# Performance work log

Measured on AMD Instinct MI355X. Metric: run time of the kernel, lower is better.

The kernel has to match this reference:

```python
import jax, jax.numpy as jnp
import numpy as np

N, E, IN, HID, H, G, CLS = 20000, 160000, 128, 96, 6, 512, 128
HD = H * HID  # heads * out_channels = 576
ARC_S = 30.0  # ArcFace scale (no margin at inference, no labels passed)


def _lin_params(key, fan_in, fan_out):
    k1, k2 = jax.random.split(key)
    lim = 1.0 / np.sqrt(fan_in)
    W = jax.random.uniform(k1, (fan_in, fan_out), minval=-lim, maxval=lim, dtype=jnp.float32)
    b = jax.random.uniform(k2, (fan_out,), minval=-lim, maxval=lim, dtype=jnp.float32)
    return W, b


def setup_inputs() -> dict:
    key = jax.random.key(0)
    ks = jax.random.split(key, 32)
    x = jax.random.normal(ks[0], (N, IN), dtype=jnp.float32)
    edge_index = jax.random.randint(ks[1], (2, E), 0, N, dtype=jnp.int64)
    batch = jnp.sort(jax.random.randint(ks[2], (N,), 0, G, dtype=jnp.int64))
    # conv1: IN -> HID (per-head dim HID, H heads)
    Wq1, bq1 = _lin_params(ks[3], IN, HD)
    Wk1, bk1 = _lin_params(ks[4], IN, HD)
    Wv1, bv1 = _lin_params(ks[5], IN, HD)
    Ws1, bs1 = _lin_params(ks[6], IN, HID)
    # convs 2..5 share shapes: HID -> HID, stacked on leading axis of 4
    def stack(fn_keys, fi, fo):
        Ws, bs = zip(*[_lin_params(k, fi, fo) for k in fn_keys])
        return jnp.stack(Ws), jnp.stack(bs)
    Wq_r, bq_r = stack(ks[7:11], HID, HD)
    Wk_r, bk_r = stack(ks[11:15], HID, HD)
    Wv_r, bv_r = stack(ks[15:19], HID, HD)
    Ws_r, bs_r = stack(ks[19:23], HID, HID)
    fc1_w, fc1_b = _lin_params(ks[23], HID, HID)
    fc2_w, fc2_b = _lin_params(ks[24], HID, HID)
    arc_w = jax.random.normal(ks[25], (CLS, HID), dtype=jnp.float32)
    return dict(x=x, edge_index=edge_index, batch=batch,
                Wq1=Wq1, bq1=bq1, Wk1=Wk1, bk1=bk1, Wv1=Wv1, bv1=bv1, Ws1=Ws1, bs1=bs1,
                Wq_r=Wq_r, bq_r=bq_r, Wk_r=Wk_r, bk_r=bk_r, Wv_r=Wv_r, bv_r=bv_r,
                Ws_r=Ws_r, bs_r=bs_r,
                fc1_w=fc1_w, fc1_b=fc1_b, fc2_w=fc2_w, fc2_b=fc2_b, arc_w=arc_w)


def transformer_conv(x, src, dst, Wq, bq, Wk, bk, Wv, bv, Ws, bs):
    n = x.shape[0]
    q = (x @ Wq + bq).reshape(n, H, HID)
    k = (x @ Wk + bk).reshape(n, H, HID)
    v = (x @ Wv + bv).reshape(n, H, HID)
    # edge-wise attention logits [E, H]
    alpha = jnp.einsum('ehd,ehd->eh', q[dst], k[src]) / jnp.sqrt(jnp.float32(HID))
    # segment softmax over incoming edges of each destination node
    m = jax.ops.segment_max(alpha, dst, num_segments=n)
    a = jnp.exp(alpha - m[dst])
    s = jax.ops.segment_sum(a, dst, num_segments=n)
    a = a / s[dst]
    out = jax.ops.segment_sum(a[:, :, None] * v[src], dst, num_segments=n)  # [n, H, HID]
    # concat=False -> mean over heads; root_weight skip connection
    return out.mean(axis=1) + x @ Ws + bs


def reference(x, edge_index, batch,
              Wq1, bq1, Wk1, bk1, Wv1, bv1, Ws1, bs1,
              Wq_r, bq_r, Wk_r, bk_r, Wv_r, bv_r, Ws_r, bs_r,
              fc1_w, fc1_b, fc2_w, fc2_b, arc_w):
    src, dst = edge_index[0], edge_index[1]
    h = jax.nn.relu(transformer_conv(x, src, dst, Wq1, bq1, Wk1, bk1, Wv1, bv1, Ws1, bs1))
    for i in range(4):  # gtconv2..gtconv5
        h = jax.nn.relu(transformer_conv(h, src, dst, Wq_r[i], bq_r[i], Wk_r[i], bk_r[i],
                                         Wv_r[i], bv_r[i], Ws_r[i], bs_r[i]))
    # global mean pool over graphs
    sums = jax.ops.segment_sum(h, batch, num_segments=G)
    cnt = jax.ops.segment_sum(jnp.ones((h.shape[0], 1), h.dtype), batch, num_segments=G)
    g = sums / jnp.maximum(cnt, 1.0)
    g = jax.nn.relu(g @ fc1_w + fc1_b)
    g = jax.nn.relu(g @ fc2_w + fc2_b)
    # ArcFace without labels: scaled cosine logits
    gn = g / (jnp.linalg.norm(g, axis=-1, keepdims=True) + 1e-12)
    wn = arc_w / (jnp.linalg.norm(arc_w, axis=-1, keepdims=True) + 1e-12)
    return ARC_S * (gn @ wn.T)
```

## Files before the change

kernel.cpp:

```cpp
#include <hip/hip_runtime.h>
#include <math.h>

#define N_NODES 20000
#define N_EDGES 160000
#define DIM_IN  128
#define HIDDEN  96
#define NH      6
#define HD      576
#define LDROW   704
#define KVF8LD  1152
#define NALL    1824
#define NGRAPH  512
#define NCLS    128
#define CHUNK   32
#define SLD     104
#define BSTR    112

typedef unsigned short ushort_t;
typedef unsigned char uchar_t;
typedef __attribute__((ext_vector_type(8))) short bf16x8;
typedef __attribute__((ext_vector_type(4))) float f32x4;
typedef __attribute__((ext_vector_type(2))) float f32x2;

static __device__ __forceinline__ ushort_t f2bf(float f) {
    unsigned int u = __float_as_uint(f);
    return (ushort_t)((u + 0x7fffu + ((u >> 16) & 1u)) >> 16);
}
static __device__ __forceinline__ float bfs(ushort_t u) { return __uint_as_float((unsigned int)u << 16); }
static __device__ __forceinline__ float bflo(unsigned int u) { return __uint_as_float(u << 16); }
static __device__ __forceinline__ float bfhi(unsigned int u) { return __uint_as_float(u & 0xffff0000u); }

#define PREP_CVT_BLOCKS 10000
#define PREP_DEG_BLOCKS 625
#define PREP_GB_BLOCKS  3
__global__ void k_prep(const float* __restrict__ x, ushort_t* __restrict__ xb,
                       const int* __restrict__ edst, int* __restrict__ deg,
                       const int* __restrict__ batch, int* __restrict__ gbound)
{
    int b = blockIdx.x;
    if (b < PREP_CVT_BLOCKS) {
        int i = b * 256 + threadIdx.x;
        if (i < N_NODES * DIM_IN) xb[i] = f2bf(x[i]);
    } else if (b < PREP_CVT_BLOCKS + PREP_DEG_BLOCKS) {
        int e = (b - PREP_CVT_BLOCKS) * 256 + threadIdx.x;
        if (e < N_EDGES) atomicAdd(&deg[edst[e]], 1);
    } else {
        int g = (b - PREP_CVT_BLOCKS - PREP_DEG_BLOCKS) * 256 + threadIdx.x;
        if (g <= NGRAPH) {
            int lo = 0, hi = N_NODES;
            while (lo < hi) {
                int mid = (lo + hi) >> 1;
                if (batch[mid] < g) lo = mid + 1; else hi = mid;
            }
            gbound[g] = lo;
        }
    }
}

__global__ void k_cvt_wT_all(
    const float* __restrict__ Wq1, const float* __restrict__ Wk1,
    const float* __restrict__ Wv1, const float* __restrict__ Ws1,
    const float* __restrict__ Wq_r, const float* __restrict__ Wk_r,
    const float* __restrict__ Wv_r, const float* __restrict__ Ws_r,
    ushort_t* __restrict__ Wb0, ushort_t* __restrict__ Wbr)
{
    const int L = blockIdx.y;
    const int K = (L == 0) ? DIM_IN : HIDDEN;
    int i = blockIdx.x * blockDim.x + threadIdx.x;
    if (i >= K * NALL) return;
    const float *Wq, *Wk, *Wv, *Ws; ushort_t* dst;
    if (L == 0) { Wq = Wq1; Wk = Wk1; Wv = Wv1; Ws = Ws1; dst = Wb0; }
    else {
        int j = L - 1;
        Wq = Wq_r + (size_t)j * HIDDEN * HD; Wk = Wk_r + (size_t)j * HIDDEN * HD;
        Wv = Wv_r + (size_t)j * HIDDEN * HD; Ws = Ws_r + (size_t)j * HIDDEN * HIDDEN;
        dst = Wbr + (size_t)j * HIDDEN * NALL;
    }
    int n = i / K, k = i - n * K;
    float v;
    if (n < 576)       v = Wq[(size_t)k * HD + n];
    else if (n < 1152) v = Wk[(size_t)k * HD + (n - 576)];
    else if (n < 1728) v = Wv[(size_t)k * HD + (n - 1152)];
    else               v = Ws[(size_t)k * HIDDEN + (n - 1728)];
    dst[i] = f2bf(v);
}

template<int KDIM>
__global__ __launch_bounds__(256) void gemm_qkvs_mfma(
    const ushort_t* __restrict__ A, int M,
    const ushort_t* __restrict__ WbT,
    const float* __restrict__ bq, const float* __restrict__ bk,
    const float* __restrict__ bv, const float* __restrict__ bs,
    ushort_t* __restrict__ kvqs, uchar_t* __restrict__ kvf8)
{
    constexpr int LDB = KDIM + 8;
    constexpr int K8  = KDIM >> 3;
    __shared__ __align__(16) ushort_t smem[128 * SLD];
    const int t    = threadIdx.x;
    const int lane = t & 63;
    const int w    = t >> 6;
    const int wm   = w & 1, wn = w >> 1;
    const int quad = lane >> 4;
    const int l16  = lane & 15;
    const int m0   = blockIdx.y * 128;
    const int rb   = blockIdx.x;
    const int n0   = rb * 96;

    for (int idx = t; idx < 96 * K8; idx += 256) {
        int c = idx / K8, kc = idx - c * K8;
        uint4 v = *(const uint4*)(WbT + (size_t)(n0 + c) * KDIM + kc * 8);
        *(uint4*)(&smem[c * LDB + kc * 8]) = v;
    }

    const ushort_t* Arow[4];
    #pragma unroll
    for (int i = 0; i < 4; i++) {
        int row = m0 + wm * 64 + i * 16 + l16;
        row = min(row, M - 1);
        Arow[i] = A + (size_t)row * KDIM + quad * 8;
    }
    __syncthreads();

    f32x4 acc[4][3] = {};
    #pragma unroll
    for (int ks = 0; ks < KDIM; ks += 32) {
        bf16x8 af[4], bfv[3];
        #pragma unroll
        for (int i = 0; i < 4; i++) af[i] = *(const bf16x8*)(Arow[i] + ks);
        #pragma unroll
        for (int j = 0; j < 3; j++)
            bfv[j] = *(const bf16x8*)(&smem[(wn * 48 + j * 16 + l16) * LDB + ks + quad * 8]);
        #pragma unroll
        for (int i = 0; i < 4; i++)
            #pragma unroll
            for (int j = 0; j < 3; j++)
                acc[i][j] = __builtin_amdgcn_mfma_f32_16x16x32_bf16(af[i], bfv[j], acc[i][j], 0, 0, 0);
    }

    int region; const float* biasp;
    if (rb < 6)       { region = 0; biasp = bq; }
    else if (rb < 12) { region = 1; biasp = bk; }
    else if (rb < 18) { region = 2; biasp = bv; }
    else              { region = 3; biasp = bs; }
    const int colbase = (region == 3) ? 0 : (rb - region * 6) * 96;
    float bj[3];
    #pragma unroll
    for (int j = 0; j < 3; j++) bj[j] = biasp[colbase + wn * 48 + j * 16 + l16];

    __syncthreads();

    if (region == 1 || region == 2) {
        uchar_t* bstage = (uchar_t*)smem;
        #pragma unroll
        for (int i = 0; i < 4; i++) {
            #pragma unroll
            for (int r = 0; r < 4; r++) {
                int row = wm * 64 + i * 16 + quad * 4 + r;
                #pragma unroll
                for (int j = 0; j < 3; j++) {
                    float v = acc[i][j][r] + bj[j];
                    int pk = __builtin_amdgcn_cvt_pk_fp8_f32(v, v, 0, false);
                    bstage[row * BSTR + wn * 48 + j * 16 + l16] = (uchar_t)(pk & 0xff);
                }
            }
        }
        __syncthreads();
        const int c0 = (rb - 6) * 96;
        for (int idx = t; idx < 128 * 6; idx += 256) {
            int r = idx / 6, v4 = idx - r * 6;
            int row = m0 + r;
            if (row < M)
                *(uint4*)(kvf8 + (size_t)row * KVF8LD + c0 + v4 * 16) =
                    *(const uint4*)(bstage + r * BSTR + v4 * 16);
        }
    } else {
        int dstoff = (region == 0) ? n0 : 576;
        #pragma unroll
        for (int i = 0; i < 4; i++) {
            #pragma unroll
            for (int r = 0; r < 4; r++) {
                int row = wm * 64 + i * 16 + quad * 4 + r;
                #pragma unroll
                for (int j = 0; j < 3; j++)
                    smem[row * SLD + wn * 48 + j * 16 + l16] = f2bf(acc[i][j][r] + bj[j]);
            }
        }
        __syncthreads();
        for (int idx = t; idx < 128 * 12; idx += 256) {
            int r = idx / 12, v = idx - r * 12;
            int row = m0 + r;
            if (row < M)
                *(uint4*)(kvqs + (size_t)row * LDROW + dstoff + v * 8) =
                    *(const uint4*)(&smem[r * SLD + v * 8]);
        }
    }
}

__global__ __launch_bounds__(1024) void k_scan(const int* __restrict__ deg,
                                               int* __restrict__ row_ptr,
                                               int* __restrict__ cursor)
{
    __shared__ int part[1024];
    int t = threadIdx.x;
    const int chunk = (N_NODES + 1023) / 1024;
    int b = t * chunk;
    int s = 0;
    for (int i = 0; i < chunk; i++)
        if (b + i < N_NODES) s += deg[b + i];
    part[t] = s;
    __syncthreads();
    for (int o = 1; o < 1024; o <<= 1) {
        int v = (t >= o) ? part[t - o] : 0;
        __syncthreads();
        part[t] += v;
        __syncthreads();
    }
    int run = part[t] - s;
    for (int i = 0; i < chunk; i++) {
        if (b + i < N_NODES) {
            row_ptr[b + i] = run;
            cursor[b + i]  = run;
            run += deg[b + i];
        }
    }
    if (t == 1023) row_ptr[N_NODES] = part[1023];
}

__global__ void k_scatter(const int* __restrict__ esrc, const int* __restrict__ edst,
                          int* __restrict__ cursor, int* __restrict__ csrc)
{
    int e = blockIdx.x * blockDim.x + threadIdx.x;
    if (e < N_EDGES) {
        int pos = atomicAdd(&cursor[edst[e]], 1);
        csrc[pos] = esrc[e];
    }
}

__global__ __launch_bounds__(64) void node_attn(
    const ushort_t* __restrict__ kvqs, const uchar_t* __restrict__ kvf8,
    const int* __restrict__ row_ptr, const int* __restrict__ csrc,
    ushort_t* __restrict__ hb)
{
    const int n    = blockIdx.x;
    const int lane = threadIdx.x;

    __shared__ float QA[HD];
    __shared__ float wbuf[CHUNK * NH];
    __shared__ int   srcs[CHUNK];
    __shared__ float mh[NH], lh[NH], scl[NH], linv[NH];

    const int beg = row_ptr[n], end = row_ptr[n + 1];
    const ushort_t* qk = kvqs + (size_t)n * LDROW;

    {
        uint4 v = *(const uint4*)(qk + lane * 8);
        unsigned int uu[4] = {v.x, v.y, v.z, v.w};
        #pragma unroll
        for (int j = 0; j < 4; j++) {
            QA[lane * 8 + 2 * j]     = bflo(uu[j]);
            QA[lane * 8 + 2 * j + 1] = bfhi(uu[j]);
        }
        if (lane < 8) {
            uint4 v2 = *(const uint4*)(qk + (64 + lane) * 8);
            unsigned int uu2[4] = {v2.x, v2.y, v2.z, v2.w};
            #pragma unroll
            for (int j = 0; j < 4; j++) {
                QA[(64 + lane) * 8 + 2 * j]     = bflo(uu2[j]);
                QA[(64 + lane) * 8 + 2 * j + 1] = bfhi(uu2[j]);
            }
        }
    }
    if (lane < NH) { mh[lane] = -1e30f; lh[lane] = 0.f; }

    const int sub = lane >> 5;
    const int h32 = lane & 31;
    const int g   = h32 >> 2;
    const int gg  = (g < 6) ? g : 0;
    const int qr  = h32 & 3;
    const int hh  = lane >> 3;
    const int j8  = lane & 7;
    const uchar_t* vb = kvf8 + 576 + ((hh < 6) ? hh : 0) * HIDDEN + j8 * 12;

    float acc[12];
    #pragma unroll
    for (int d = 0; d < 12; d++) acc[d] = 0.f;
    const float qa = 0.10206207261596577f;

    __syncthreads();

    for (int cb = beg; cb < end; cb += CHUNK) {
        const int c = min(CHUNK, end - cb);
        if (lane < c) srcs[lane] = csrc[cb + lane];
        __syncthreads();

        #pragma unroll 2
        for (int eb = 0; eb < c; eb += 2) {
            int e = eb + sub;
            bool act = (e < c) && (g < 6);
            int src = srcs[(e < c) ? e : 0];
            const uchar_t* kp = kvf8 + (size_t)src * KVF8LD + gg * HIDDEN + qr * 24;
            uint2 a0 = *(const uint2*)(kp);
            uint2 a1 = *(const uint2*)(kp + 8);
            uint2 a2 = *(const uint2*)(kp + 16);
            const float* qb = &QA[gg * HIDDEN + qr * 24];
            unsigned int uu[6] = {a0.x, a0.y, a1.x, a1.y, a2.x, a2.y};
            float p = 0.f;
            #pragma unroll
            for (int k2 = 0; k2 < 6; k2++) {
                f32x2 lo = __builtin_amdgcn_cvt_pk_f32_fp8(uu[k2], false);
                f32x2 hi = __builtin_amdgcn_cvt_pk_f32_fp8(uu[k2], true);
                p += lo[0] * qb[4 * k2]     + lo[1] * qb[4 * k2 + 1]
                   + hi[0] * qb[4 * k2 + 2] + hi[1] * qb[4 * k2 + 3];
            }
            p += __shfl_xor(p, 1, 64);
            p += __shfl_xor(p, 2, 64);
            if (act && qr == 0) wbuf[e * NH + g] = p * qa;
        }
        __syncthreads();

        #pragma unroll
        for (int s = 0; s < 3; s++) {
            int h = 2 * s + sub;
            float logit = (h32 < c) ? wbuf[h32 * NH + h] : -1e30f;
            float cm = logit;
            #pragma unroll
            for (int o = 16; o; o >>= 1) cm = fmaxf(cm, __shfl_xor(cm, o, 32));
            cm = fmaxf(cm, mh[h]);
            float wv = (h32 < c) ? __expf(logit - cm) : 0.f;
            if (h32 < c) wbuf[h32 * NH + h] = wv;
            float lp = wv;
            #pragma unroll
            for (int o = 16; o; o >>= 1) lp += __shfl_xor(lp, o, 32);
            if (h32 == 0) {
                float sc = __expf(mh[h] - cm);
                scl[h] = sc;
                lh[h] = lh[h] * sc + lp;
                mh[h] = cm;
            }
        }
        __syncthreads();

        if (lane < 48) {
            float sc = scl[hh];
            #pragma unroll
            for (int d = 0; d < 12; d++) acc[d] *= sc;
            int e = 0;
            for (; e + 2 <= c; e += 2) {
                int s0 = srcs[e], s1 = srcs[e + 1];
                const uchar_t* p0 = vb + (size_t)s0 * KVF8LD;
                const uchar_t* p1 = vb + (size_t)s1 * KVF8LD;
                unsigned int r0[3], r1[3];
                #pragma unroll
                for (int k = 0; k < 3; k++) {
                    r0[k] = *(const unsigned int*)(p0 + 4 * k);
                    r1[k] = *(const unsigned int*)(p1 + 4 * k);
                }
                float w0 = wbuf[e * NH + hh], w1 = wbuf[(e + 1) * NH + hh];
                #pragma unroll
                for (int k = 0; k < 3; k++) {
                    f32x2 lo0 = __builtin_amdgcn_cvt_pk_f32_fp8(r0[k], false);
                    f32x2 hi0 = __builtin_amdgcn_cvt_pk_f32_fp8(r0[k], true);
                    acc[4 * k]     += w0 * lo0[0];
                    acc[4 * k + 1] += w0 * lo0[1];
                    acc[4 * k + 2] += w0 * hi0[0];
                    acc[4 * k + 3] += w0 * hi0[1];
                    f32x2 lo1 = __builtin_amdgcn_cvt_pk_f32_fp8(r1[k], false);
                    f32x2 hi1 = __builtin_amdgcn_cvt_pk_f32_fp8(r1[k], true);
                    acc[4 * k]     += w1 * lo1[0];
                    acc[4 * k + 1] += w1 * lo1[1];
                    acc[4 * k + 2] += w1 * hi1[0];
                    acc[4 * k + 3] += w1 * hi1[1];
                }
            }
            if (e < c) {
                int s0 = srcs[e];
                const uchar_t* p0 = vb + (size_t)s0 * KVF8LD;
                float w0 = wbuf[e * NH + hh];
                #pragma unroll
                for (int k = 0; k < 3; k++) {
                    unsigned int r = *(const unsigned int*)(p0 + 4 * k);
                    f32x2 lo = __builtin_amdgcn_cvt_pk_f32_fp8(r, false);
                    f32x2 hi = __builtin_amdgcn_cvt_pk_f32_fp8(r, true);
                    acc[4 * k]     += w0 * lo[0];
                    acc[4 * k + 1] += w0 * lo[1];
                    acc[4 * k + 2] += w0 * hi[0];
                    acc[4 * k + 3] += w0 * hi[1];
                }
            }
        }
        __syncthreads();
    }

    if (lane < NH) linv[lane] = (lh[lane] > 0.f) ? 1.0f / lh[lane] : 0.f;
    __syncthreads();
    if (lane < 48) {
        float li = linv[hh];
        #pragma unroll
        for (int d = 0; d < 12; d++)
            QA[hh * HIDDEN + j8 * 12 + d] = acc[d] * li;
    }
    __syncthreads();

    {
        int d = lane;
        float s = (QA[d] + QA[HIDDEN + d] + QA[2 * HIDDEN + d] +
                   QA[3 * HIDDEN + d] + QA[4 * HIDDEN + d] + QA[5 * HIDDEN + d])
                  * (1.0f / 6.0f);
        s += bfs(qk[576 + d]);
        s = fmaxf(s, 0.0f);
        hb[n * HIDDEN + d] = f2bf(s);
        if (lane < 32) {
            int d2 = 64 + lane;
            float s2 = (QA[d2] + QA[HIDDEN + d2] + QA[2 * HIDDEN + d2] +
                        QA[3 * HIDDEN + d2] + QA[4 * HIDDEN + d2] + QA[5 * HIDDEN + d2])
                       * (1.0f / 6.0f);
            s2 += bfs(qk[576 + d2]);
            s2 = fmaxf(s2, 0.0f);
            hb[n * HIDDEN + d2] = f2bf(s2);
        }
    }
}

__global__ __launch_bounds__(128) void k_head(
    const ushort_t* __restrict__ hb, const int* __restrict__ gbound,
    const float* __restrict__ fc1w, const float* __restrict__ fc1b,
    const float* __restrict__ fc2w, const float* __restrict__ fc2b,
    const float* __restrict__ arcw, float* __restrict__ out)
{
    int g = blockIdx.x, t = threadIdx.x;
    __shared__ float v0[HIDDEN], v1[HIDDEN], v2[HIDDEN];
    __shared__ float gnorm;
    const int s0 = gbound[g], s1 = gbound[g + 1];
    float cnt = fmaxf((float)(s1 - s0), 1.0f);
    if (t < HIDDEN) {
        float s = 0.f;
        for (int n = s0; n < s1; n++) s += bfs(hb[(size_t)n * HIDDEN + t]);
        v0[t] = s / cnt;
    }
    __syncthreads();
    if (t < HIDDEN) {
        float s = fc1b[t];
        for (int k = 0; k < HIDDEN; k++) s += v0[k] * fc1w[k * HIDDEN + t];
        v1[t] = fmaxf(s, 0.f);
    }
    __syncthreads();
    if (t < HIDDEN) {
        float s = fc2b[t];
        for (int k = 0; k < HIDDEN; k++) s += v1[k] * fc2w[k * HIDDEN + t];
        v2[t] = fmaxf(s, 0.f);
    }
    __syncthreads();
    if (t == 0) {
        float s = 0.f;
        for (int k = 0; k < HIDDEN; k++) s += v2[k] * v2[k];
        gnorm = sqrtf(s) + 1e-12f;
    }
    __syncthreads();
    if (t < NCLS) {
        float dot = 0.f, wn = 0.f;
        const float* wr = arcw + (size_t)t * HIDDEN;
        for (int k = 0; k < HIDDEN; k++) {
            float w = wr[k];
            dot += w * v2[k];
            wn  += w * w;
        }
        out[g * NCLS + t] = 30.0f * dot / (gnorm * (sqrtf(wn) + 1e-12f));
    }
}

extern "C" void kernel_launch(void* const* d_in, const int* in_sizes, int n_in,
                              void* d_out, int out_size, void* d_ws, size_t ws_size,
                              hipStream_t stream)
{
    (void)in_sizes; (void)n_in; (void)out_size; (void)ws_size;

    const float* x     = (const float*)d_in[0];
    const int*   ei    = (const int*)d_in[1];
    const int*   batch = (const int*)d_in[2];
    const float* Wq1 = (const float*)d_in[3];  const float* bq1 = (const float*)d_in[4];
    const float* Wk1 = (const float*)d_in[5];  const float* bk1 = (const float*)d_in[6];
    const float* Wv1 = (const float*)d_in[7];  const float* bv1 = (const float*)d_in[8];
    const float* Ws1 = (const float*)d_in[9];  const float* bs1 = (const float*)d_in[10];
    const float* Wq_r = (const float*)d_in[11]; const float* bq_r = (const float*)d_in[12];
    const float* Wk_r = (const float*)d_in[13]; const float* bk_r = (const float*)d_in[14];
    const float* Wv_r = (const float*)d_in[15]; const float* bv_r = (const float*)d_in[16];
    const float* Ws_r = (const float*)d_in[17]; const float* bs_r = (const float*)d_in[18];
    const float* fc1w = (const float*)d_in[19]; const float* fc1b = (const float*)d_in[20];
    const float* fc2w = (const float*)d_in[21]; const float* fc2b = (const float*)d_in[22];
    const float* arcw = (const float*)d_in[23];
    float* out = (float*)d_out;

    const int* esrc = ei;
    const int* edst = ei + N_EDGES;

    char* base = (char*)d_ws;
    size_t off = 0;
    auto alloc = [&](size_t bytes) -> void* {
        off = (off + 255) & ~(size_t)255;
        void* p = base + off;
        off += bytes;
        return p;
    };
    ushort_t* kvqs = (ushort_t*)alloc((size_t)N_NODES * LDROW * 2);
    uchar_t*  kvf8 = (uchar_t*)alloc((size_t)N_NODES * KVF8LD);
    ushort_t* xb  = (ushort_t*)alloc((size_t)N_NODES * DIM_IN * 2);
    ushort_t* hb0 = (ushort_t*)alloc((size_t)N_NODES * HIDDEN * 2);
    ushort_t* hb1 = (ushort_t*)alloc((size_t)N_NODES * HIDDEN * 2);
    ushort_t* Wb0 = (ushort_t*)alloc((size_t)DIM_IN * NALL * 2);
    ushort_t* Wbr = (ushort_t*)alloc((size_t)4 * HIDDEN * NALL * 2);
    int*   deg     = (int*)alloc(N_NODES * 4);
    int*   row_ptr = (int*)alloc((N_NODES + 1) * 4);
    int*   cursor  = (int*)alloc(N_NODES * 4);
    int*   csrc    = (int*)alloc(N_EDGES * 4);
    int*   gbound  = (int*)alloc((NGRAPH + 1) * 4);

    hipMemsetAsync(deg, 0, N_NODES * 4, stream);
    k_prep<<<PREP_CVT_BLOCKS + PREP_DEG_BLOCKS + PREP_GB_BLOCKS, 256, 0, stream>>>(
        x, xb, edst, deg, batch, gbound);
    {
        dim3 gw((DIM_IN * NALL + 255) / 256, 5);
        k_cvt_wT_all<<<gw, 256, 0, stream>>>(Wq1, Wk1, Wv1, Ws1,
                                             Wq_r, Wk_r, Wv_r, Ws_r, Wb0, Wbr);
    }
    k_scan<<<1, 1024, 0, stream>>>(deg, row_ptr, cursor);
    k_scatter<<<(N_EDGES + 255) / 256, 256, 0, stream>>>(esrc, edst, cursor, csrc);

    const ushort_t* Ain = xb;
    ushort_t* hbcur = hb0;
    for (int L = 0; L < 5; L++) {
        const ushort_t* Wb = (L == 0) ? Wb0 : (Wbr + (size_t)(L - 1) * HIDDEN * NALL);
        const float *bq, *bk, *bv, *bs;
        if (L == 0) { bq = bq1; bk = bk1; bv = bv1; bs = bs1; }
        else {
            int i = L - 1;
            bq = bq_r + (size_t)i * HD; bk = bk_r + (size_t)i * HD;
            bv = bv_r + (size_t)i * HD; bs = bs_r + (size_t)i * HIDDEN;
        }
        dim3 g(19, (N_NODES + 127) / 128);
        if (L == 0)
            gemm_qkvs_mfma<DIM_IN><<<g, 256, 0, stream>>>(Ain, N_NODES, Wb,
                                                          bq, bk, bv, bs, kvqs, kvf8);
        else
            gemm_qkvs_mfma<HIDDEN><<<g, 256, 0, stream>>>(Ain, N_NODES, Wb,
                                                          bq, bk, bv, bs, kvqs, kvf8);
        node_attn<<<N_NODES, 64, 0, stream>>>(kvqs, kvf8, row_ptr, csrc, hbcur);
        Ain = hbcur;
        hbcur = (hbcur == hb0) ? hb1 : hb0;
    }

    k_head<<<NGRAPH, 128, 0, stream>>>(hbcur == hb0 ? hb1 : hb0, gbound,
                                       fc1w, fc1b, fc2w, fc2b, arcw, out);
}
```

Measured before the change: 511.7 us.

## Keep query slice in registers and prefetch first eight V rows before logits

Each lane now loads its own 24-element query slice straight into registers instead of staging the whole query row through shared memory, which removes LDS reads from the logit inner loop. For every chunk, the first eight edges' V fp8 data is loaded into registers before the logit and softmax phases so that the gather latency overlaps that compute. The aggregation loop then starts from edge 8. This raises register pressure by roughly 48 VGPRs per lane, which may reduce occupancy, and it issues redundant clamped loads when a chunk has fewer than eight edges.

```diff
diff --git a/kernel.cpp b/kernel.cpp
--- a/kernel.cpp
+++ b/kernel.cpp
@@ -244,33 +244,13 @@
     const int n    = blockIdx.x;
     const int lane = threadIdx.x;
 
-    __shared__ float QA[HD];
     __shared__ float wbuf[CHUNK * NH];
     __shared__ int   srcs[CHUNK];
     __shared__ float mh[NH], lh[NH], scl[NH], linv[NH];
+    __shared__ float arr[HD];
 
     const int beg = row_ptr[n], end = row_ptr[n + 1];
     const ushort_t* qk = kvqs + (size_t)n * LDROW;
-
-    {
-        uint4 v = *(const uint4*)(qk + lane * 8);
-        unsigned int uu[4] = {v.x, v.y, v.z, v.w};
-        #pragma unroll
-        for (int j = 0; j < 4; j++) {
-            QA[lane * 8 + 2 * j]     = bflo(uu[j]);
-            QA[lane * 8 + 2 * j + 1] = bfhi(uu[j]);
-        }
-        if (lane < 8) {
-            uint4 v2 = *(const uint4*)(qk + (64 + lane) * 8);
-            unsigned int uu2[4] = {v2.x, v2.y, v2.z, v2.w};
-            #pragma unroll
-            for (int j = 0; j < 4; j++) {
-                QA[(64 + lane) * 8 + 2 * j]     = bflo(uu2[j]);
-                QA[(64 + lane) * 8 + 2 * j + 1] = bfhi(uu2[j]);
-            }
-        }
-    }
-    if (lane < NH) { mh[lane] = -1e30f; lh[lane] = 0.f; }
 
     const int sub = lane >> 5;
     const int h32 = lane & 31;
@@ -281,6 +261,23 @@
     const int j8  = lane & 7;
     const uchar_t* vb = kvf8 + 576 + ((hh < 6) ? hh : 0) * HIDDEN + j8 * 12;
 
+    float qv[24];
+    {
+        const ushort_t* qp = qk + gg * HIDDEN + qr * 24;
+        uint4 q0 = *(const uint4*)(qp);
+        uint4 q1 = *(const uint4*)(qp + 8);
+        uint4 q2 = *(const uint4*)(qp + 16);
+        unsigned int qq[12] = {q0.x, q0.y, q0.z, q0.w,
+                               q1.x, q1.y, q1.z, q1.w,
+                               q2.x, q2.y, q2.z, q2.w};
+        #pragma unroll
+        for (int j = 0; j < 12; j++) {
+            qv[2 * j]     = bflo(qq[j]);
+            qv[2 * j + 1] = bfhi(qq[j]);
+        }
+    }
+    if (lane < NH) { mh[lane] = -1e30f; lh[lane] = 0.f; }
+
     float acc[12];
     #pragma unroll
     for (int d = 0; d < 12; d++) acc[d] = 0.f;
@@ -292,6 +289,18 @@
         const int c = min(CHUNK, end - cb);
         if (lane < c) srcs[lane] = csrc[cb + lane];
         __syncthreads();
+
+        unsigned int vpre[24];
+        if (lane < 48) {
+            #pragma unroll
+            for (int j = 0; j < 8; j++) {
+                int e = min(j, c - 1);
+                const uchar_t* p = vb + (size_t)srcs[e] * KVF8LD;
+                #pragma unroll
+                for (int k = 0; k < 3; k++)
+                    vpre[j * 3 + k] = *(const unsigned int*)(p + 4 * k);
+            }
+        }
 
         #pragma unroll 2
         for (int eb = 0; eb < c; eb += 2) {
@@ -302,15 +311,14 @@
             uint2 a0 = *(const uint2*)(kp);
             uint2 a1 = *(const uint2*)(kp + 8);
             uint2 a2 = *(const uint2*)(kp + 16);
-            const float* qb = &QA[gg * HIDDEN + qr * 24];
             unsigned int uu[6] = {a0.x, a0.y, a1.x, a1.y, a2.x, a2.y};
             float p = 0.f;
             #pragma unroll
             for (int k2 = 0; k2 < 6; k2++) {
                 f32x2 lo = __builtin_amdgcn_cvt_pk_f32_fp8(uu[k2], false);
                 f32x2 hi = __builtin_amdgcn_cvt_pk_f32_fp8(uu[k2], true);
-                p += lo[0] * qb[4 * k2]     + lo[1] * qb[4 * k2 + 1]
-                   + hi[0] * qb[4 * k2 + 2] + hi[1] * qb[4 * k2 + 3];
+                p += lo[0] * qv[4 * k2]     + lo[1] * qv[4 * k2 + 1]
+                   + hi[0] * qv[4 * k2 + 2] + hi[1] * qv[4 * k2 + 3];
             }
             p += __shfl_xor(p, 1, 64);
             p += __shfl_xor(p, 2, 64);
@@ -344,7 +352,22 @@
             float sc = scl[hh];
             #pragma unroll
             for (int d = 0; d < 12; d++) acc[d] *= sc;
-            int e = 0;
+            #pragma unroll
+            for (int j = 0; j < 8; j++) {
+                if (j < c) {
+                    float w0 = wbuf[j * NH + hh];
+                    #pragma unroll
+                    for (int k = 0; k < 3; k++) {
+                        f32x2 lo = __builtin_amdgcn_cvt_pk_f32_fp8(vpre[j * 3 + k], false);
+                        f32x2 hi = __builtin_amdgcn_cvt_pk_f32_fp8(vpre[j * 3 + k], true);
+                        acc[4 * k]     += w0 * lo[0];
+                        acc[4 * k + 1] += w0 * lo[1];
+                        acc[4 * k + 2] += w0 * hi[0];
+                        acc[4 * k + 3] += w0 * hi[1];
+                    }
+                }
+            }
+            int e = 8;
             for (; e + 2 <= c; e += 2) {
                 int s0 = srcs[e], s1 = srcs[e + 1];
                 const uchar_t* p0 = vb + (size_t)s0 * KVF8LD;
@@ -397,22 +420,22 @@
         float li = linv[hh];
         #pragma unroll
         for (int d = 0; d < 12; d++)
-            QA[hh * HIDDEN + j8 * 12 + d] = acc[d] * li;
+            arr[hh * HIDDEN + j8 * 12 + d] = acc[d] * li;
     }
     __syncthreads();
 
     {
         int d = lane;
-        float s = (QA[d] + QA[HIDDEN + d] + QA[2 * HIDDEN + d] +
-                   QA[3 * HIDDEN + d] + QA[4 * HIDDEN + d] + QA[5 * HIDDEN + d])
+        float s = (arr[d] + arr[HIDDEN + d] + arr[2 * HIDDEN + d] +
+                   arr[3 * HIDDEN + d] + arr[4 * HIDDEN + d] + arr[5 * HIDDEN + d])
                   * (1.0f / 6.0f);
         s += bfs(qk[576 + d]);
         s = fmaxf(s, 0.0f);
         hb[n * HIDDEN + d] = f2bf(s);
         if (lane < 32) {
             int d2 = 64 + lane;
-            float s2 = (QA[d2] + QA[HIDDEN + d2] + QA[2 * HIDDEN + d2] +
-                        QA[3 * HIDDEN + d2] + QA[4 * HIDDEN + d2] + QA[5 * HIDDEN + d2])
+            float s2 = (arr[d2] + arr[HIDDEN + d2] + arr[2 * HIDDEN + d2] +
+                        arr[3 * HIDDEN + d2] + arr[4 * HIDDEN + d2] + arr[5 * HIDDEN + d2])
                        * (1.0f / 6.0f);
             s2 += bfs(qk[576 + d2]);
             s2 = fmaxf(s2, 0.0f);
```

Measured after the change: 538.0 us. 5.1% more time.
